# Kernel tuning notes

Measured on AMD Instinct MI355X. Metric: run time of the kernel, lower is better.

The kernel has to match this reference:

```python
import jax, jax.numpy as jnp
import numpy as np

B, L, D = 2, 2048, 2048
H, KV, HD = 16, 8, 128
EPS = 1e-5
ROPE_BASE = 10000.0
SCALING_ALPHA = 1.0
SCALE = HD ** -0.5


def setup_inputs() -> dict:
    key = jax.random.key(0)
    ks = jax.random.split(key, 5)
    s = 0.02  # weight init scale
    return {
        "x": jax.random.normal(ks[0], (B, L, D), jnp.float32),
        "wq": jax.random.normal(ks[1], (D, H * HD), jnp.float32) * s,
        "wk": jax.random.normal(ks[2], (D, KV * HD), jnp.float32) * s,
        "wv": jax.random.normal(ks[3], (D, KV * HD), jnp.float32) * s,
        "wo": jax.random.normal(ks[4], (H * HD, D), jnp.float32) * s,
        "qn_w": jnp.ones((HD,), jnp.float32),
        "kn_w": jnp.ones((HD,), jnp.float32),
    }


def _rope(t):
    # t: [B, h, L, HD]. DynamicNTKAlpha base scaling (alpha=1 -> no-op).
    base = ROPE_BASE * SCALING_ALPHA ** (HD / (HD - 2))
    # NOTE: source uses base**(+i/d) (no negative exponent) -- kept faithful.
    freqs = base ** (jnp.arange(0, HD, 2, dtype=jnp.float32) / HD)  # [HD/2]
    pos = jnp.arange(t.shape[-2], dtype=jnp.float32)                # [L]
    angles = pos[:, None] * freqs[None, :]                          # [L, HD/2]
    cos, sin = jnp.cos(angles), jnp.sin(angles)
    x1, x2 = t[..., : HD // 2], t[..., HD // 2 :]
    return jnp.concatenate([x1 * cos - x2 * sin, x2 * cos + x1 * sin], axis=-1)


def _rmsnorm(t, w):
    return t * jax.lax.rsqrt(jnp.mean(t * t, axis=-1, keepdims=True) + EPS) * w


def reference(x, wq, wk, wv, wo, qn_w, kn_w):
    b, l, _ = x.shape
    q = (x @ wq).reshape(b, l, H, HD).transpose(0, 2, 1, 3)   # [B,H,L,HD]
    k = (x @ wk).reshape(b, l, KV, HD).transpose(0, 2, 1, 3)  # [B,KV,L,HD]
    v = (x @ wv).reshape(b, l, KV, HD).transpose(0, 2, 1, 3)
    q = _rmsnorm(_rope(q), qn_w)
    k = _rmsnorm(_rope(k), kn_w)
    # GQA: expand KV heads to match query heads
    rep = H // KV
    k = jnp.repeat(k, rep, axis=1)  # [B,H,L,HD]
    v = jnp.repeat(v, rep, axis=1)
    scores = jnp.einsum("bhqd,bhkd->bhqk", q, k) * SCALE
    probs = jax.nn.softmax(scores, axis=-1)
    out = jnp.einsum("bhqk,bhkd->bhqd", probs, v)             # [B,H,L,HD]
    out = out.transpose(0, 2, 1, 3).reshape(b, l, H * HD)
    return out @ wo
```

## Files before the change

kernel.cpp:

```cpp
#include <hip/hip_runtime.h>
#include <math.h>

#define BB 2
#define LL 2048
#define DD 2048
#define HH 16
#define KVH 8
#define HDIM 128
#define SCALE_F 0.08838834764831845f
#define EPS_F 1e-5f
#define LOG2E 1.4426950408889634f
#define SMAX_F 17.0f
#define QKVW 4096

typedef unsigned short u16;
typedef __attribute__((ext_vector_type(8))) short short8;
typedef __attribute__((ext_vector_type(4))) float f32x4;
typedef __attribute__((ext_vector_type(16))) float f32x16;

#define MFMA16(a, b, c) __builtin_amdgcn_mfma_f32_16x16x32_bf16((a), (b), (c), 0, 0, 0)
#define MFMA32(a, b, c) __builtin_amdgcn_mfma_f32_32x32x16_bf16((a), (b), (c), 0, 0, 0)

__device__ __forceinline__ float b2f(u16 u) {
    union { unsigned int i; float f; } x;
    x.i = ((unsigned int)u) << 16;
    return x.f;
}
__device__ __forceinline__ u16 f2b(float f) {
    unsigned int x = __float_as_uint(f);
    unsigned int r = x + 0x7FFFu + ((x >> 16) & 1u);
    return (u16)(r >> 16);
}
__device__ __forceinline__ u16 f2b_fast(float f) {
    return (u16)((__float_as_uint(f) + 0x8000u) >> 16);
}
__device__ __forceinline__ void g2l(const u16* g, u16* l) {
    __builtin_amdgcn_global_load_lds(
        (const __attribute__((address_space(1))) unsigned int*)g,
        (__attribute__((address_space(3))) unsigned int*)l, 16, 0, 0);
}

__global__ __launch_bounds__(256) void prep_kernel(const float* __restrict__ x,
                                                   u16* __restrict__ xb,
                                                   const float* __restrict__ wq,
                                                   const float* __restrict__ wk,
                                                   const float* __restrict__ wv,
                                                   const float* __restrict__ wo,
                                                   u16* __restrict__ wqkvT,
                                                   u16* __restrict__ woT,
                                                   float* __restrict__ ct,
                                                   float* __restrict__ st) {
    __shared__ u16 t[64 * 65];
    const int blk = blockIdx.x, tid = threadIdx.x;
    if (blk < 8192) {
        int i = (blk * 256 + tid) * 4;
        float4 v = *(const float4*)(x + i);
        unsigned int p0 = (unsigned int)f2b(v.x) | ((unsigned int)f2b(v.y) << 16);
        unsigned int p1 = (unsigned int)f2b(v.z) | ((unsigned int)f2b(v.w) << 16);
        uint2 pk; pk.x = p0; pk.y = p1;
        *(uint2*)(xb + i) = pk;
    } else if (blk < 11264) {
        int j = blk - 8192;
        const float* in; u16* out; int C, bx, by;
        if (j < 1024)      { in = wq; out = wqkvT;                      C = 2048; bx = j & 31; by = j >> 5; }
        else if (j < 1536) { j -= 1024; in = wk; out = wqkvT + (size_t)2048 * DD; C = 1024; bx = j & 15; by = j >> 4; }
        else if (j < 2048) { j -= 1536; in = wv; out = wqkvT + (size_t)3072 * DD; C = 1024; bx = j & 15; by = j >> 4; }
        else               { j -= 2048; in = wo; out = woT;                      C = 2048; bx = j & 31; by = j >> 5; }
        int c0 = bx * 64, r0 = by * 64;
#pragma unroll
        for (int i = 0; i < 16; i++) {
            int idx = tid + i * 256;
            int r = idx >> 6, c = idx & 63;
            t[r * 65 + c] = f2b(in[(size_t)(r0 + r) * C + c0 + c]);
        }
        __syncthreads();
#pragma unroll
        for (int i = 0; i < 16; i++) {
            int idx = tid + i * 256;
            int r = idx >> 6, c = idx & 63;
            out[(size_t)(c0 + r) * DD + r0 + c] = t[c * 65 + r];
        }
    } else {
        int i = (blk - 11264) * 256 + tid;
        int pos = i >> 6, d = i & 63;
        float freq = (float)pow(10000.0, (double)d * (1.0 / 64.0));
        float ang = (float)pos * freq;
        double a = (double)ang;
        ct[i] = (float)cos(a);
        st[i] = (float)sin(a);
    }
}

__global__ __launch_bounds__(256) void gemm_bt(const u16* __restrict__ A,
                                               const u16* __restrict__ Bt,
                                               u16* __restrict__ C, int M, int N, int K) {
    __shared__ __align__(16) u16 As[128 * 64];
    __shared__ __align__(16) u16 Bs[128 * 64];
    const int tid = threadIdx.x;
    const int w = tid >> 6, lane = tid & 63;
    const int lm = lane & 15, lq = lane >> 4;
    const int bn0 = blockIdx.x * 128, bm0 = blockIdx.y * 128;
    const int wm = (w >> 1) * 64, wn = (w & 1) * 64;

    f32x4 acc[4][4];
#pragma unroll
    for (int i = 0; i < 4; i++)
#pragma unroll
        for (int j = 0; j < 4; j++) acc[i][j] = (f32x4){0.f, 0.f, 0.f, 0.f};

    const int srow = lane >> 3;
    const int sgr = (lane & 7) ^ (srow & 7);
    const u16* ga = A + (size_t)(bm0 + w * 32 + srow) * K + sgr * 8;
    const u16* gb = Bt + (size_t)(bn0 + w * 32 + srow) * K + sgr * 8;
    u16* lA = &As[(w * 32) * 64];
    u16* lB = &Bs[(w * 32) * 64];

    for (int k0 = 0; k0 < K; k0 += 64) {
        __syncthreads();
#pragma unroll
        for (int ch = 0; ch < 4; ch++)
            g2l(ga + (size_t)(ch * 8) * K + k0, lA + ch * 8 * 64);
#pragma unroll
        for (int ch = 0; ch < 4; ch++)
            g2l(gb + (size_t)(ch * 8) * K + k0, lB + ch * 8 * 64);
        __syncthreads();

#pragma unroll
        for (int sub = 0; sub < 2; sub++) {
            short8 af[4], bf[4];
#pragma unroll
            for (int mt = 0; mt < 4; mt++) {
                int row = wm + mt * 16 + lm;
                af[mt] = *(const short8*)(&As[row * 64 + ((sub * 4 + lq) ^ (lm & 7)) * 8]);
            }
#pragma unroll
            for (int nt = 0; nt < 4; nt++) {
                int row = wn + nt * 16 + lm;
                bf[nt] = *(const short8*)(&Bs[row * 64 + ((sub * 4 + lq) ^ (lm & 7)) * 8]);
            }
#pragma unroll
            for (int mt = 0; mt < 4; mt++)
#pragma unroll
                for (int nt = 0; nt < 4; nt++) acc[mt][nt] = MFMA16(af[mt], bf[nt], acc[mt][nt]);
        }
    }

#pragma unroll
    for (int mt = 0; mt < 4; mt++)
#pragma unroll
        for (int nt = 0; nt < 4; nt++)
#pragma unroll
            for (int r = 0; r < 4; r++) {
                int row = bm0 + wm + mt * 16 + lq * 4 + r;
                int col = bn0 + wn + nt * 16 + lm;
                C[(size_t)row * N + col] = f2b(acc[mt][nt][r]);
            }
}

__global__ __launch_bounds__(256) void gemm_bt_o(const u16* __restrict__ A,
                                                 const u16* __restrict__ Bt,
                                                 float* __restrict__ C, int M, int N, int K) {
    __shared__ __align__(16) u16 As[64 * 64];
    __shared__ __align__(16) u16 Bs[128 * 64];
    const int tid = threadIdx.x;
    const int w = tid >> 6, lane = tid & 63;
    const int lm = lane & 15, lq = lane >> 4;
    const int bn0 = blockIdx.x * 128, bm0 = blockIdx.y * 64;
    const int wm = (w >> 1) * 32, wn = (w & 1) * 64;

    f32x4 acc[2][4];
#pragma unroll
    for (int i = 0; i < 2; i++)
#pragma unroll
        for (int j = 0; j < 4; j++) acc[i][j] = (f32x4){0.f, 0.f, 0.f, 0.f};

    const int srow = lane >> 3;
    const int sgr = (lane & 7) ^ (srow & 7);
    const u16* ga = A + (size_t)(bm0 + w * 16 + srow) * K + sgr * 8;
    const u16* gb = Bt + (size_t)(bn0 + w * 32 + srow) * K + sgr * 8;
    u16* lA = &As[(w * 16) * 64];
    u16* lB = &Bs[(w * 32) * 64];

    for (int k0 = 0; k0 < K; k0 += 64) {
        __syncthreads();
#pragma unroll
        for (int ch = 0; ch < 2; ch++)
            g2l(ga + (size_t)(ch * 8) * K + k0, lA + ch * 8 * 64);
#pragma unroll
        for (int ch = 0; ch < 4; ch++)
            g2l(gb + (size_t)(ch * 8) * K + k0, lB + ch * 8 * 64);
        __syncthreads();

#pragma unroll
        for (int sub = 0; sub < 2; sub++) {
            short8 af[2], bf[4];
#pragma unroll
            for (int mt = 0; mt < 2; mt++) {
                int row = wm + mt * 16 + lm;
                af[mt] = *(const short8*)(&As[row * 64 + ((sub * 4 + lq) ^ (lm & 7)) * 8]);
            }
#pragma unroll
            for (int nt = 0; nt < 4; nt++) {
                int row = wn + nt * 16 + lm;
                bf[nt] = *(const short8*)(&Bs[row * 64 + ((sub * 4 + lq) ^ (lm & 7)) * 8]);
            }
#pragma unroll
            for (int mt = 0; mt < 2; mt++)
#pragma unroll
                for (int nt = 0; nt < 4; nt++) acc[mt][nt] = MFMA16(af[mt], bf[nt], acc[mt][nt]);
        }
    }

#pragma unroll
    for (int mt = 0; mt < 2; mt++)
#pragma unroll
        for (int nt = 0; nt < 4; nt++)
#pragma unroll
            for (int r = 0; r < 4; r++) {
                int row = bm0 + wm + mt * 16 + lq * 4 + r;
                int col = bn0 + wn + nt * 16 + lm;
                C[(size_t)row * N + col] = acc[mt][nt][r];
            }
}

__global__ __launch_bounds__(256) void ropetv_kernel(u16* __restrict__ qkv,
                                                     u16* __restrict__ vt,
                                                     const float* __restrict__ qw,
                                                     const float* __restrict__ kw,
                                                     const float* __restrict__ ct,
                                                     const float* __restrict__ st) {
    __shared__ u16 t[64 * 65];
    const int blk = blockIdx.x, tid = threadIdx.x;
    if (blk < 24576) {
        int slot = blk * 4 + (tid >> 6);
        int lane = tid & 63;
        int hh = slot % (HH + KVH);
        int row = slot / (HH + KVH);
        int pos = row & (LL - 1);

        u16* base = qkv + (size_t)row * QKVW + hh * HDIM;
        const float* w = (hh < HH) ? qw : kw;

        float x1 = b2f(base[lane]), x2 = b2f(base[lane + 64]);
        float c = ct[pos * 64 + lane], s = st[pos * 64 + lane];
        float r1 = x1 * c - x2 * s;
        float r2 = x2 * c + x1 * s;
        float ss = r1 * r1 + r2 * r2;
#pragma unroll
        for (int m = 1; m < 64; m <<= 1) ss += __shfl_xor(ss, m, 64);
        float sc = 1.0f / sqrtf(ss * (1.0f / 128.0f) + EPS_F);
        base[lane] = f2b(r1 * sc * w[lane]);
        base[lane + 64] = f2b(r2 * sc * w[lane + 64]);
    } else {
        int j = blk - 24576;
        int bx = j & 31, by = (j >> 5) & 1, bg = j >> 6;
        int l0 = bx * 64, d0 = by * 64;
        int b = bg >> 3, g = bg & 7;
        const u16* src = qkv + (size_t)b * LL * QKVW + 3072 + g * HDIM;
        u16* dst = vt + (size_t)bg * HDIM * LL;
#pragma unroll
        for (int i = 0; i < 16; i++) {
            int idx = tid + i * 256;
            int r = idx >> 6, c = idx & 63;
            t[r * 65 + c] = src[(size_t)(l0 + r) * QKVW + d0 + c];
        }
        __syncthreads();
#pragma unroll
        for (int i = 0; i < 16; i++) {
            int idx = tid + i * 256;
            int r = idx >> 6, c = idx & 63;
            dst[(size_t)(d0 + r) * LL + l0 + c] = t[c * 65 + r];
        }
    }
}

__global__ __launch_bounds__(256, 2) void attn_kernel(const u16* __restrict__ qkv,
                                                      const u16* __restrict__ vt,
                                                      u16* __restrict__ ob) {
    __shared__ __align__(16) u16 Kt[64 * 128];
    __shared__ __align__(16) u16 Vt[128 * 64];
    __shared__ __align__(16) u16 Ps[4][32 * 64];

    const int tid = threadIdx.x, w = tid >> 6, lane = tid & 63;
    const int l31 = lane & 31, lh = lane >> 5;
    const int q0 = blockIdx.x * 128;
    const int bh = blockIdx.y, b = bh >> 4, hd = bh & 15, g = hd >> 1;

    const u16* kbase = qkv + (size_t)b * LL * QKVW + 2048 + g * HDIM;
    const u16* vtbase = vt + (size_t)(b * KVH + g) * HDIM * LL;

    const int krl = lane >> 4, kgl = lane & 15;
    const int vrl = lane >> 3, vgl = lane & 7;

    const int qrow = q0 + w * 32 + l31;
    short8 aq[8];
    {
        const u16* qp = qkv + (size_t)(b * LL + qrow) * QKVW + hd * HDIM + lh * 8;
#pragma unroll
        for (int kk = 0; kk < 8; kk++) aq[kk] = *(const short8*)(qp + kk * 16);
    }

    f32x16 o[4];
#pragma unroll
    for (int i = 0; i < 4; i++)
#pragma unroll
        for (int r = 0; r < 16; r++) o[i][r] = 0.f;
    float psum[16];
#pragma unroll
    for (int r = 0; r < 16; r++) psum[r] = 0.f;
    const float SC2 = SCALE_F * LOG2E;

    for (int t = 0; t < LL / 64; t++) {
        __syncthreads();
#pragma unroll
        for (int ch = 0; ch < 4; ch++) {
            int r = w * 16 + ch * 4 + krl;
            int gc = kgl ^ (r & 15);
            g2l(kbase + (size_t)(t * 64 + r) * QKVW + gc * 8,
                &Kt[(w * 16 + ch * 4) * 128]);
        }
#pragma unroll
        for (int ch = 0; ch < 4; ch++) {
            int r = w * 32 + ch * 8 + vrl;
            int gc = vgl ^ (r & 7);
            g2l(vtbase + (size_t)r * LL + t * 64 + gc * 8,
                &Vt[(w * 32 + ch * 8) * 64]);
        }
        __syncthreads();

        f32x16 s[2];
#pragma unroll
        for (int kt = 0; kt < 2; kt++) {
#pragma unroll
            for (int r = 0; r < 16; r++) s[kt][r] = 0.f;
            int key = kt * 32 + l31;
#pragma unroll
            for (int kk = 0; kk < 8; kk++) {
                int gg = (kk * 2 + lh) ^ (key & 15);
                short8 bf = *(const short8*)(&Kt[key * 128 + gg * 8]);
                s[kt] = MFMA32(aq[kk], bf, s[kt]);
            }
        }

#pragma unroll
        for (int kt = 0; kt < 2; kt++) {
            int key = kt * 32 + l31;
#pragma unroll
            for (int r = 0; r < 16; r++) {
                float p = exp2f(fmaf(s[kt][r], SC2, -SMAX_F));
                psum[r] += p;
                int row = (r & 3) + 8 * (r >> 2) + 4 * lh;
                Ps[w][row * 64 + (key ^ ((row & 7) << 3))] = f2b_fast(p);
            }
        }
        __syncthreads();

#pragma unroll
        for (int kc = 0; kc < 4; kc++) {
            int gp = ((kc * 2 + lh) ^ (l31 & 7)) * 8;
            short8 pa = *(const short8*)(&Ps[w][l31 * 64 + gp]);
#pragma unroll
            for (int dn = 0; dn < 4; dn++) {
                int d = dn * 32 + l31;
                int gv = ((kc * 2 + lh) ^ (d & 7)) * 8;
                short8 bv = *(const short8*)(&Vt[d * 64 + gv]);
                o[dn] = MFMA32(pa, bv, o[dn]);
            }
        }
    }

#pragma unroll
    for (int m = 1; m < 32; m <<= 1)
#pragma unroll
        for (int r = 0; r < 16; r++) psum[r] += __shfl_xor(psum[r], m, 32);
    float inv[16];
#pragma unroll
    for (int r = 0; r < 16; r++) inv[r] = 1.0f / psum[r];

    u16* obase = ob + (size_t)(b * LL + q0 + w * 32) * (HH * HDIM) + hd * HDIM;
#pragma unroll
    for (int dn = 0; dn < 4; dn++)
#pragma unroll
        for (int r = 0; r < 16; r++) {
            int row = (r & 3) + 8 * (r >> 2) + 4 * lh;
            obase[(size_t)row * (HH * HDIM) + dn * 32 + l31] = f2b(o[dn][r] * inv[r]);
        }
}

extern "C" void kernel_launch(void* const* d_in, const int* in_sizes, int n_in,
                              void* d_out, int out_size, void* d_ws, size_t ws_size,
                              hipStream_t stream) {
    const float* x  = (const float*)d_in[0];
    const float* wq = (const float*)d_in[1];
    const float* wk = (const float*)d_in[2];
    const float* wv = (const float*)d_in[3];
    const float* wo = (const float*)d_in[4];
    const float* qn = (const float*)d_in[5];
    const float* kn = (const float*)d_in[6];

    u16* ws = (u16*)d_ws;
    const size_t SZ_X = (size_t)BB * LL * DD;
    u16* xb    = ws;
    u16* qkv   = xb + SZ_X;
    u16* wqkvT = qkv + (size_t)BB * LL * QKVW;
    u16* woT   = wqkvT + (size_t)QKVW * DD;
    float* ct  = (float*)(woT + (size_t)DD * DD);
    float* st  = ct + (size_t)LL * 64;
    u16* att = xb;
    u16* vt  = wqkvT;

    prep_kernel<<<dim3(11776), dim3(256), 0, stream>>>(x, xb, wq, wk, wv, wo,
                                                       wqkvT, woT, ct, st);
    gemm_bt<<<dim3(QKVW / 128, BB * LL / 128), dim3(256), 0, stream>>>(xb, wqkvT, qkv, BB * LL, QKVW, DD);
    ropetv_kernel<<<dim3(25600), dim3(256), 0, stream>>>(qkv, vt, qn, kn, ct, st);
    attn_kernel<<<dim3(LL / 128, BB * HH), dim3(256), 0, stream>>>(qkv, vt, att);
    gemm_bt_o<<<dim3(DD / 128, BB * LL / 64), dim3(256), 0, stream>>>(att, woT, (float*)d_out, BB * LL, DD, DD);
}
```

Measured before the change: 366.0 us.

## Double-buffer K/V tiles and keep P in registers via transposed QK^T

Double-buffers the K and V LDS tiles so the next tile's global-to-LDS load is issued while the current tile is computed, cutting the per-iteration syncs from three to one. The QK^T MFMA operands are swapped so each lane holds one query row's scores; P is converted with v_cvt_pk_bf16_f32 and rearranged with v_permlane32_swap into PV A-operands, which removes the P round trip through LDS and a barrier. The row sum becomes a single scalar per lane and is broadcast at the end, and s_setprio is raised around the MFMA sections. LDS use doubles, which could lower occupancy, and the register-level P layout depends on the exact semantics of the permlane swap.

```diff
diff --git a/kernel.cpp b/kernel.cpp
--- a/kernel.cpp
+++ b/kernel.cpp
@@ -31,8 +31,13 @@
     unsigned int r = x + 0x7FFFu + ((x >> 16) & 1u);
     return (u16)(r >> 16);
 }
-__device__ __forceinline__ u16 f2b_fast(float f) {
-    return (u16)((__float_as_uint(f) + 0x8000u) >> 16);
+__device__ __forceinline__ unsigned cvtpk(float lo, float hi) {
+    unsigned r;
+    asm("v_cvt_pk_bf16_f32 %0, %1, %2" : "=v"(r) : "v"(lo), "v"(hi));
+    return r;
+}
+__device__ __forceinline__ void pl32swap(unsigned &a, unsigned &b) {
+    asm("v_permlane32_swap_b32 %0, %1" : "+v"(a), "+v"(b));
 }
 __device__ __forceinline__ void g2l(const u16* g, u16* l) {
     __builtin_amdgcn_global_load_lds(
@@ -277,9 +282,8 @@
 __global__ __launch_bounds__(256, 2) void attn_kernel(const u16* __restrict__ qkv,
                                                       const u16* __restrict__ vt,
                                                       u16* __restrict__ ob) {
-    __shared__ __align__(16) u16 Kt[64 * 128];
-    __shared__ __align__(16) u16 Vt[128 * 64];
-    __shared__ __align__(16) u16 Ps[4][32 * 64];
+    __shared__ __align__(16) u16 Kt[2][64 * 128];
+    __shared__ __align__(16) u16 Vt[2][128 * 64];
 
     const int tid = threadIdx.x, w = tid >> 6, lane = tid & 63;
     const int l31 = lane & 31, lh = lane >> 5;
@@ -292,6 +296,23 @@
     const int krl = lane >> 4, kgl = lane & 15;
     const int vrl = lane >> 3, vgl = lane & 7;
 
+#define STAGE(tt, bi) do {                                                   \
+        _Pragma("unroll")                                                    \
+        for (int ch = 0; ch < 4; ch++) {                                     \
+            int r_ = w * 16 + ch * 4 + krl;                                  \
+            int gc_ = kgl ^ (r_ & 15);                                       \
+            g2l(kbase + (size_t)((tt) * 64 + r_) * QKVW + gc_ * 8,           \
+                &Kt[bi][(w * 16 + ch * 4) * 128]);                           \
+        }                                                                    \
+        _Pragma("unroll")                                                    \
+        for (int ch = 0; ch < 4; ch++) {                                     \
+            int r_ = w * 32 + ch * 8 + vrl;                                  \
+            int gc_ = vgl ^ (r_ & 7);                                        \
+            g2l(vtbase + (size_t)r_ * LL + (tt) * 64 + gc_ * 8,              \
+                &Vt[bi][(w * 32 + ch * 8) * 64]);                            \
+        }                                                                    \
+    } while (0)
+
     const int qrow = q0 + w * 32 + l31;
     short8 aq[8];
     {
@@ -305,77 +326,85 @@
     for (int i = 0; i < 4; i++)
 #pragma unroll
         for (int r = 0; r < 16; r++) o[i][r] = 0.f;
-    float psum[16];
-#pragma unroll
-    for (int r = 0; r < 16; r++) psum[r] = 0.f;
+    float psum = 0.f;
     const float SC2 = SCALE_F * LOG2E;
 
+    STAGE(0, 0);
+    __syncthreads();
+
+    int cur = 0;
     for (int t = 0; t < LL / 64; t++) {
-        __syncthreads();
-#pragma unroll
-        for (int ch = 0; ch < 4; ch++) {
-            int r = w * 16 + ch * 4 + krl;
-            int gc = kgl ^ (r & 15);
-            g2l(kbase + (size_t)(t * 64 + r) * QKVW + gc * 8,
-                &Kt[(w * 16 + ch * 4) * 128]);
-        }
-#pragma unroll
-        for (int ch = 0; ch < 4; ch++) {
-            int r = w * 32 + ch * 8 + vrl;
-            int gc = vgl ^ (r & 7);
-            g2l(vtbase + (size_t)r * LL + t * 64 + gc * 8,
-                &Vt[(w * 32 + ch * 8) * 64]);
-        }
-        __syncthreads();
+        if (t + 1 < LL / 64) STAGE(t + 1, cur ^ 1);
 
         f32x16 s[2];
 #pragma unroll
+        for (int kt = 0; kt < 2; kt++)
+#pragma unroll
+            for (int r = 0; r < 16; r++) s[kt][r] = 0.f;
+        __builtin_amdgcn_s_setprio(1);
+#pragma unroll
+        for (int kk = 0; kk < 8; kk++) {
+#pragma unroll
+            for (int kt = 0; kt < 2; kt++) {
+                int key = kt * 32 + l31;
+                int gg = (kk * 2 + lh) ^ (key & 15);
+                short8 kf = *(const short8*)(&Kt[cur][key * 128 + gg * 8]);
+                s[kt] = MFMA32(kf, aq[kk], s[kt]);
+            }
+        }
+        __builtin_amdgcn_s_setprio(0);
+
+        unsigned pw[4][4];
+#pragma unroll
         for (int kt = 0; kt < 2; kt++) {
-#pragma unroll
-            for (int r = 0; r < 16; r++) s[kt][r] = 0.f;
-            int key = kt * 32 + l31;
-#pragma unroll
-            for (int kk = 0; kk < 8; kk++) {
-                int gg = (kk * 2 + lh) ^ (key & 15);
-                short8 bf = *(const short8*)(&Kt[key * 128 + gg * 8]);
-                s[kt] = MFMA32(aq[kk], bf, s[kt]);
-            }
-        }
-
-#pragma unroll
-        for (int kt = 0; kt < 2; kt++) {
-            int key = kt * 32 + l31;
+            float p[16];
 #pragma unroll
             for (int r = 0; r < 16; r++) {
-                float p = exp2f(fmaf(s[kt][r], SC2, -SMAX_F));
-                psum[r] += p;
-                int row = (r & 3) + 8 * (r >> 2) + 4 * lh;
-                Ps[w][row * 64 + (key ^ ((row & 7) << 3))] = f2b_fast(p);
-            }
-        }
-        __syncthreads();
-
+                p[r] = exp2f(fmaf(s[kt][r], SC2, -SMAX_F));
+                psum += p[r];
+            }
+#pragma unroll
+            for (int half = 0; half < 2; half++) {
+                int kc = kt * 2 + half, qb = half * 8;
+                unsigned c0 = cvtpk(p[qb + 0], p[qb + 1]);
+                unsigned c1 = cvtpk(p[qb + 2], p[qb + 3]);
+                unsigned c2 = cvtpk(p[qb + 4], p[qb + 5]);
+                unsigned c3 = cvtpk(p[qb + 6], p[qb + 7]);
+                pl32swap(c0, c2);
+                pl32swap(c1, c3);
+                pw[kc][0] = c0; pw[kc][1] = c1; pw[kc][2] = c2; pw[kc][3] = c3;
+            }
+        }
+
+        __builtin_amdgcn_s_setprio(1);
 #pragma unroll
         for (int kc = 0; kc < 4; kc++) {
-            int gp = ((kc * 2 + lh) ^ (l31 & 7)) * 8;
-            short8 pa = *(const short8*)(&Ps[w][l31 * 64 + gp]);
+            union { unsigned u[4]; short8 s8; } pu;
+#pragma unroll
+            for (int i = 0; i < 4; i++) pu.u[i] = pw[kc][i];
 #pragma unroll
             for (int dn = 0; dn < 4; dn++) {
                 int d = dn * 32 + l31;
                 int gv = ((kc * 2 + lh) ^ (d & 7)) * 8;
-                short8 bv = *(const short8*)(&Vt[d * 64 + gv]);
-                o[dn] = MFMA32(pa, bv, o[dn]);
-            }
-        }
-    }
-
-#pragma unroll
-    for (int m = 1; m < 32; m <<= 1)
-#pragma unroll
-        for (int r = 0; r < 16; r++) psum[r] += __shfl_xor(psum[r], m, 32);
-    float inv[16];
-#pragma unroll
-    for (int r = 0; r < 16; r++) inv[r] = 1.0f / psum[r];
+                short8 bv = *(const short8*)(&Vt[cur][d * 64 + gv]);
+                o[dn] = MFMA32(pu.s8, bv, o[dn]);
+            }
+        }
+        __builtin_amdgcn_s_setprio(0);
+
+        __syncthreads();
+        cur ^= 1;
+    }
+#undef STAGE
+
+    psum += __shfl_xor(psum, 32, 64);
+    float inv = 1.0f / psum;
+    float invr[16];
+#pragma unroll
+    for (int r = 0; r < 16; r++) {
+        int row = (r & 3) + 8 * (r >> 2) + 4 * lh;
+        invr[r] = __shfl(inv, row, 32);
+    }
 
     u16* obase = ob + (size_t)(b * LL + q0 + w * 32) * (HH * HDIM) + hd * HDIM;
 #pragma unroll
@@ -383,7 +412,7 @@
 #pragma unroll
         for (int r = 0; r < 16; r++) {
             int row = (r & 3) + 8 * (r >> 2) + 4 * lh;
-            obase[(size_t)row * (HH * HDIM) + dn * 32 + l31] = f2b(o[dn][r] * inv[r]);
+            obase[(size_t)row * (HH * HDIM) + dn * 32 + l31] = f2b(o[dn][r] * invr[r]);
         }
 }
 
```

After: 362.7 us. No clear change (-0.9%).
